# Performance work log

Hardware: AMD Instinct MI355X
Metric: run time of the kernel (lower is better)

## Reference

```python
import jax, jax.numpy as jnp
import numpy as np

K = 9          # kernel_size (number of KNN neighbours), dilation=1
SCALAR = 20.0  # scalar in _build_explain
EPS = 1e-10


def setup_inputs() -> dict:
    key = jax.random.key(0)
    ks = jax.random.split(key, 9)
    B, C, H, W = 16, 192, 28, 28
    Cout, r = 384, 16
    f = lambda k, s, sc: jax.random.normal(k, s, jnp.float32) * sc
    return {
        "x": f(ks[0], (B, C, H, W), 1.0),
        "w_edge": f(ks[1], (Cout, 2 * C), 0.05),  # 1x1 conv on concat[x_i, x_j-x_i]
        "b_edge": f(ks[2], (Cout,), 0.05),
        "w1": f(ks[3], (C // r, C), 0.1),          # CBAM channel MLP (shared)
        "b1": f(ks[4], (C // r,), 0.1),
        "w2": f(ks[5], (C, C // r), 0.1),
        "b2": f(ks[6], (C,), 0.1),
        "w_sp": f(ks[7], (1, 2, 7, 7), 0.1),       # CBAM spatial 7x7 conv
        "b_sp": f(ks[8], (1,), 0.1),
    }


def _cbam(x, w1, b1, w2, b2, w_sp, b_sp):
    # Standard CBAM: channel gate (avg+max pooled -> shared MLP -> sigmoid)
    # then spatial gate (channel mean/max -> 7x7 conv -> sigmoid).
    mlp = lambda v: jax.nn.relu(v @ w1.T + b1) @ w2.T + b2
    ch = jax.nn.sigmoid(mlp(x.mean((2, 3))) + mlp(x.max((2, 3))))
    x = x * ch[:, :, None, None]
    sp_in = jnp.stack([x.mean(1), x.max(1)], axis=1)  # (B,2,H,W)
    sp = jax.lax.conv_general_dilated(sp_in, w_sp, (1, 1), [(3, 3), (3, 3)])
    return x * jax.nn.sigmoid(sp + b_sp[None, :, None, None])


def _build_explain(att_x):
    B, C, H, W = att_x.shape
    a = jax.nn.softmax(att_x.reshape(B, C, H * W), axis=2)
    a = a / (a.max(axis=2, keepdims=True) + EPS)
    return (2.0 * a - 1.0) / (2.0 * SCALAR) + 1.0  # (B,C,N)


def _knn_idx(xf):
    # DenseDilatedKnnGraph: L2-normalize over channels, pairwise sq-dist, topk.
    xn = xf / jnp.maximum(jnp.linalg.norm(xf, axis=1, keepdims=True), 1e-12)
    xt = jnp.swapaxes(xn, 1, 2)                      # (B,N,C)
    sq = jnp.sum(xt * xt, axis=-1)                   # (B,N)
    dist = sq[:, :, None] - 2.0 * jnp.einsum("bnc,bmc->bnm", xt, xt) + sq[:, None, :]
    _, idx = jax.lax.top_k(-dist, K)                 # nn_idx = edge_index[0], (B,N,K)
    return idx


def reference(x, w_edge, b_edge, w1, b1, w2, b2, w_sp, b_sp):
    B, C, H, W = x.shape
    N = H * W
    xf = x.reshape(B, C, N)
    idx = _knn_idx(xf)                               # dynamic KNN graph (B,N,K)
    att = _build_explain(_cbam(x, w1, b1, w2, b2, w_sp, b_sp))
    xf = xf * att
    # EdgeConv2d: x_i = center (edge_index[1] is arange -> broadcast),
    # x_j gathered by neighbour indices.
    x_i = xf[:, :, :, None]                           # (B,C,N,1)
    x_e = jnp.broadcast_to(x_i, (B, C, N, K))
    i_e = jnp.broadcast_to(idx[:, None, :, :], (B, C, N, K))
    x_j = jnp.take_along_axis(x_e, i_e, axis=2)       # (B,C,N,K)
    feat = jnp.concatenate([x_e, x_j - x_i], axis=1)  # (B,2C,N,K)
    out = jnp.einsum("oc,bcnk->bonk", w_edge, feat) + b_edge[None, :, None, None]
    out = jax.nn.relu(out)                            # BasicConv: 1x1 conv + relu
    out = out.max(axis=-1)                            # max over neighbours (B,O,N)
    return out.reshape(B, -1, H, W)
```

## Files before the change

### kernel.cpp

```cpp
#include <hip/hip_runtime.h>
#include <math.h>

#define HW 784
#define Cc 192
#define Bb 16
#define CO 384
#define KK 9
#define OG 8

typedef __attribute__((ext_vector_type(8))) short bf16x8;
typedef __attribute__((ext_vector_type(4))) float f32x4;

__device__ __forceinline__ unsigned f2ord(float f){
  unsigned u = __float_as_uint(f);
  return (u & 0x80000000u) ? ~u : (u | 0x80000000u);
}

__device__ __forceinline__ unsigned short b16rne(float v){
  unsigned u = __float_as_uint(v);
  unsigned r = u + 0x7FFFu + ((u >> 16) & 1u);
  return (unsigned short)(r >> 16);
}

__global__ void k_chstats(const float* __restrict__ x, float* __restrict__ chm, float* __restrict__ chx){
  int wid = threadIdx.x >> 6, lane = threadIdx.x & 63;
  int r = blockIdx.x * 4 + wid;
  const float* row = x + (size_t)r * HW;
  float s = 0.f, m = -3.4e38f;
  for (int n = lane; n < HW; n += 64){ float v = row[n]; s += v; m = fmaxf(m, v); }
  for (int off = 32; off; off >>= 1){ s += __shfl_xor(s, off); m = fmaxf(m, __shfl_xor(m, off)); }
  if (lane == 0){ chm[r] = s / (float)HW; chx[r] = m; }
}

__global__ void k_mlp(const float* __restrict__ chm, const float* __restrict__ chx,
                      const float* __restrict__ w1, const float* __restrict__ b1,
                      const float* __restrict__ w2, const float* __restrict__ b2,
                      float* __restrict__ chv){
  int b = blockIdx.x, t = threadIdx.x;
  __shared__ float vm[Cc], vx[Cc], hp[2][12];
  if (t < Cc){ vm[t] = chm[b*Cc + t]; vx[t] = chx[b*Cc + t]; }
  __syncthreads();
  if (t < 24){
    int h = t % 12;
    const float* src = (t < 12) ? vm : vx;
    float a = b1[h];
    for (int c = 0; c < Cc; ++c) a += src[c] * w1[h*Cc + c];
    hp[t/12][h] = fmaxf(a, 0.f);
  }
  __syncthreads();
  if (t < Cc){
    float a = 2.f * b2[t];
    for (int h = 0; h < 12; ++h) a += (hp[0][h] + hp[1][h]) * w2[t*12 + h];
    chv[b*Cc + t] = 1.f / (1.f + expf(-a));
  }
}

__global__ void k_spin(const float* __restrict__ x, const float* __restrict__ chv,
                       float* __restrict__ amean, float* __restrict__ amax,
                       float* __restrict__ nrm){
  int b = blockIdx.x >> 2;
  int n = ((blockIdx.x & 3) << 8) + threadIdx.x;
  if (n >= HW) return;
  const float* xb = x + (size_t)b*Cc*HW + n;
  const float* cb = chv + b*Cc;
  float s = 0.f, m = -3.4e38f, sq = 0.f;
  for (int c = 0; c < Cc; ++c){
    float xv = xb[(size_t)c*HW];
    float v = xv * cb[c];
    s += v; m = fmaxf(m, v); sq += xv*xv;
  }
  amean[b*HW + n] = s / (float)Cc;
  amax[b*HW + n]  = m;
  nrm[b*HW + n]   = fmaxf(sqrtf(sq), 1e-12f);
}

__global__ void k_conv(const float* __restrict__ amean, const float* __restrict__ amax,
                       const float* __restrict__ wsp, const float* __restrict__ bsp,
                       float* __restrict__ satt){
  int b = blockIdx.x >> 2;
  int n = ((blockIdx.x & 3) << 8) + threadIdx.x;
  if (n >= HW) return;
  int yy = n / 28, xx = n % 28;
  float a = 0.f;
  for (int ky = 0; ky < 7; ++ky){
    int iy = yy + ky - 3; if (iy < 0 || iy >= 28) continue;
    for (int kx = 0; kx < 7; ++kx){
      int ix = xx + kx - 3; if (ix < 0 || ix >= 28) continue;
      int ii = b*HW + iy*28 + ix;
      a += amean[ii]*wsp[ky*7 + kx] + amax[ii]*wsp[49 + ky*7 + kx];
    }
  }
  satt[b*HW + n] = 1.f / (1.f + expf(-(a + bsp[0])));
}

__global__ void k_attstats(const float* __restrict__ x, const float* __restrict__ chv,
                           const float* __restrict__ satt,
                           float* __restrict__ vmaxA, float* __restrict__ invA){
  int wid = threadIdx.x >> 6, lane = threadIdx.x & 63;
  int r = blockIdx.x * 4 + wid;
  int b = r / Cc;
  const float* row = x + (size_t)r * HW;
  const float* sr = satt + b * HW;
  float ch = chv[r];
  float vv[13];
  float m = -3.4e38f;
  #pragma unroll
  for (int i = 0; i < 13; ++i){
    int n = lane + 64*i;
    vv[i] = (n < HW) ? (row[n] * ch) * sr[n] : -3.4e38f;
    m = fmaxf(m, vv[i]);
  }
  for (int off = 32; off; off >>= 1) m = fmaxf(m, __shfl_xor(m, off));
  float s = 0.f;
  #pragma unroll
  for (int i = 0; i < 13; ++i){
    int n = lane + 64*i;
    if (n < HW) s += expf(vv[i] - m);
  }
  for (int off = 32; off; off >>= 1) s += __shfl_xor(s, off);
  if (lane == 0){ vmaxA[r] = m; invA[r] = 1.f / (1.f + 1e-10f * s); }
}

__global__ __launch_bounds__(256) void k_cvt2(const float* __restrict__ x, const float* __restrict__ nrm,
                                              const float* __restrict__ chv, const float* __restrict__ satt,
                                              const float* __restrict__ vmaxA, const float* __restrict__ invA,
                                              unsigned short* __restrict__ Xnh, unsigned short* __restrict__ Xnl,
                                              unsigned short* __restrict__ XAh, unsigned short* __restrict__ XAl){
  int b = blockIdx.z, c0 = blockIdx.y*64, n0 = blockIdx.x*64;
  __shared__ float T[64][65];
  __shared__ float chs[64], vms[64], ivs[64];
  int t = threadIdx.x;
  int nl = (t & 15) * 4, cl = t >> 4;
  const float* xb = x + (size_t)b*Cc*HW;
  #pragma unroll
  for (int r = 0; r < 4; ++r){
    int c_loc = cl + r*16;
    int n = n0 + nl;
    float4 v = (n < HW) ? *(const float4*)(xb + (size_t)(c0 + c_loc)*HW + n) : make_float4(0,0,0,0);
    *(float4*)&T[c_loc][nl] = v;
  }
  if (t < 64){
    chs[t] = chv[b*Cc + c0 + t];
    vms[t] = vmaxA[b*Cc + c0 + t];
    ivs[t] = invA[b*Cc + c0 + t];
  }
  __syncthreads();
  int nr = t >> 2, q = t & 3;
  int n_g = n0 + nr;
  if (n_g >= HW) return;
  float nv = nrm[b*HW + n_g];
  float sr = satt[b*HW + n_g];
  unsigned int nh[8], nlw[8], ah[8], al[8];
  #pragma unroll
  for (int j = 0; j < 8; ++j){
    unsigned int parts[2][2];
    #pragma unroll
    for (int e = 0; e < 2; ++e){
      int cc_ = q*16 + 2*j + e;
      float v = T[cc_][nr];
      float xnv = v / nv;
      unsigned short h0 = b16rne(xnv);
      float l0 = xnv - __uint_as_float((unsigned)h0 << 16);
      parts[0][e] = (unsigned)h0 | ((unsigned)b16rne(l0) << 16);
      float vvv = (v * chs[cc_]) * sr;
      float ex = expf(vvv - vms[cc_]);
      float a = ex * ivs[cc_];
      float xav = v * ((2.f*a - 1.f)*0.025f + 1.f);
      unsigned short h1 = b16rne(xav);
      float l1 = xav - __uint_as_float((unsigned)h1 << 16);
      parts[1][e] = (unsigned)h1 | ((unsigned)b16rne(l1) << 16);
    }
    nh[j]  = (parts[0][0] & 0xFFFFu) | (parts[0][1] << 16);
    nlw[j] = (parts[0][0] >> 16)     | (parts[0][1] & 0xFFFF0000u);
    ah[j]  = (parts[1][0] & 0xFFFFu) | (parts[1][1] << 16);
    al[j]  = (parts[1][0] >> 16)     | (parts[1][1] & 0xFFFF0000u);
  }
  size_t base = ((size_t)b*HW + n_g)*Cc + c0 + q*16;
  *(uint4*)(Xnh + base)     = make_uint4(nh[0], nh[1], nh[2], nh[3]);
  *(uint4*)(Xnh + base + 8) = make_uint4(nh[4], nh[5], nh[6], nh[7]);
  *(uint4*)(Xnl + base)     = make_uint4(nlw[0], nlw[1], nlw[2], nlw[3]);
  *(uint4*)(Xnl + base + 8) = make_uint4(nlw[4], nlw[5], nlw[6], nlw[7]);
  *(uint4*)(XAh + base)     = make_uint4(ah[0], ah[1], ah[2], ah[3]);
  *(uint4*)(XAh + base + 8) = make_uint4(ah[4], ah[5], ah[6], ah[7]);
  *(uint4*)(XAl + base)     = make_uint4(al[0], al[1], al[2], al[3]);
  *(uint4*)(XAl + base + 8) = make_uint4(al[4], al[5], al[6], al[7]);
}

__global__ __launch_bounds__(256) void k_gram(const unsigned short* __restrict__ Xth,
                                              const unsigned short* __restrict__ Xtl,
                                              float* __restrict__ D){
  int b = blockIdx.z;
  int n0 = blockIdx.y*128, m0 = blockIdx.x*128;
  __shared__ unsigned short Als[8192];
  __shared__ unsigned short Bls[8192];
  int t = threadIdx.x, w = t >> 6, l = t & 63;
  int wr = w >> 1, wc = w & 1;
  f32x4 acc[4][4] = {};
  int nn = t >> 1, half = t & 1;
  size_t bb = (size_t)b*HW*Cc;
  int ra = n0 + nn; if (ra > HW-1) ra = HW-1;
  int rb = m0 + nn; if (rb > HW-1) rb = HW-1;

  for (int cc = 0; cc < 9; ++cc){
    int seg = cc/3, kc0 = (cc%3)*64;
    const unsigned short* As_ = (seg < 2 ? Xth : Xtl) + bb;
    const unsigned short* Bs_ = (seg == 1 ? Xtl : Xth) + bb;
    const uint4* ga = (const uint4*)(As_ + (size_t)ra*Cc + kc0 + half*32);
    const uint4* gb = (const uint4*)(Bs_ + (size_t)rb*Cc + kc0 + half*32);
    uint4 va0 = ga[0], va1 = ga[1], va2 = ga[2], va3 = ga[3];
    uint4 vb0 = gb[0], vb1 = gb[1], vb2 = gb[2], vb3 = gb[3];
    __syncthreads();
    int base = nn*128 + half*64;
    int sw = (nn & 7) << 4;
    *(uint4*)((char*)Als + ((base      ) ^ sw)) = va0;
    *(uint4*)((char*)Als + ((base + 16 ) ^ sw)) = va1;
    *(uint4*)((char*)Als + ((base + 32 ) ^ sw)) = va2;
    *(uint4*)((char*)Als + ((base + 48 ) ^ sw)) = va3;
    *(uint4*)((char*)Bls + ((base      ) ^ sw)) = vb0;
    *(uint4*)((char*)Bls + ((base + 16 ) ^ sw)) = vb1;
    *(uint4*)((char*)Bls + ((base + 32 ) ^ sw)) = vb2;
    *(uint4*)((char*)Bls + ((base + 48 ) ^ sw)) = vb3;
    __syncthreads();
    #pragma unroll
    for (int ks = 0; ks < 2; ++ks){
      bf16x8 af[4], bfr[4];
      int kb = ks*64 + (l >> 4)*16;
      #pragma unroll
      for (int mt = 0; mt < 4; ++mt){
        int rl = wr*64 + mt*16 + (l & 15);
        int off = (rl*128 + kb) ^ ((rl & 7) << 4);
        af[mt] = *(const bf16x8*)((const char*)Als + off);
      }
      #pragma unroll
      for (int nt = 0; nt < 4; ++nt){
        int cl2 = wc*64 + nt*16 + (l & 15);
        int off = (cl2*128 + kb) ^ ((cl2 & 7) << 4);
        bfr[nt] = *(const bf16x8*)((const char*)Bls + off);
      }
      #pragma unroll
      for (int mt = 0; mt < 4; ++mt)
        #pragma unroll
        for (int nt = 0; nt < 4; ++nt)
          acc[mt][nt] = __builtin_amdgcn_mfma_f32_16x16x32_bf16(af[mt], bfr[nt], acc[mt][nt], 0, 0, 0);
    }
  }
  #pragma unroll
  for (int mt = 0; mt < 4; ++mt){
    #pragma unroll
    for (int nt = 0; nt < 4; ++nt){
      int col = m0 + wc*64 + nt*16 + (l & 15);
      if (col >= HW) continue;
      int row0 = n0 + wr*64 + mt*16 + ((l >> 4) << 2);
      #pragma unroll
      for (int r = 0; r < 4; ++r){
        int row = row0 + r;
        if (row < HW) D[((size_t)b*HW + row)*HW + col] = -acc[mt][nt][r];
      }
    }
  }
}

__global__ __launch_bounds__(256) void k_select(const float* __restrict__ D, int* __restrict__ idxo){
  int wid = threadIdx.x >> 6, lane = threadIdx.x & 63;
  int row = blockIdx.x * 4 + wid;
  const float* Dr = D + (size_t)row * HW;
  float dvv[13]; int mvv[13];
  #pragma unroll
  for (int i = 0; i < 13; ++i){
    int m = lane + 64*i;
    dvv[i] = (m < HW) ? Dr[m] : 3.4e38f;
    mvv[i] = m;
  }
  for (int k = 0; k < KK; ++k){
    float bd = dvv[0]; int bi = 0;
    #pragma unroll
    for (int i = 1; i < 13; ++i) if (dvv[i] < bd){ bd = dvv[i]; bi = i; }
    unsigned long long key = ((unsigned long long)f2ord(bd) << 32) | (unsigned)mvv[bi];
    for (int off = 32; off; off >>= 1){
      unsigned long long o = __shfl_xor(key, off);
      if (o < key) key = o;
    }
    int wm = (int)(unsigned)(key & 0xffffffffu);
    if (lane == 0) idxo[(size_t)k*(Bb*HW) + row] = wm;
    if (mvv[bi] == wm) dvv[bi] = 3.4e38f;
  }
}

__global__ void k_wp(const float* __restrict__ we, unsigned short* __restrict__ Wph,
                     unsigned short* __restrict__ Wpl){
  int i = blockIdx.x*256 + threadIdx.x;
  if (i >= 768*Cc) return;
  int o = i / Cc, c = i % Cc;
  float v = (o < CO) ? (we[(size_t)o*384 + c] - we[(size_t)o*384 + Cc + c])
                     : we[(size_t)(o - CO)*384 + Cc + c];
  unsigned short h = b16rne(v);
  float lo = v - __uint_as_float((unsigned)h << 16);
  Wph[i] = h;
  Wpl[i] = b16rne(lo);
}

__global__ __launch_bounds__(256) void k_gemm2(const unsigned short* __restrict__ Wph,
                                               const unsigned short* __restrict__ Wpl,
                                               const unsigned short* __restrict__ XAh,
                                               const unsigned short* __restrict__ XAl,
                                               float* __restrict__ PQ){
  int b = blockIdx.z;
  int o0 = blockIdx.y*128, n0 = blockIdx.x*128;
  __shared__ unsigned short Als[8192];
  __shared__ unsigned short Bls[8192];
  int t = threadIdx.x, w = t >> 6, l = t & 63;
  int wr = w >> 1, wc = w & 1;
  f32x4 acc[4][4] = {};
  int nn = t >> 1, half = t & 1;
  size_t bx = (size_t)b*HW*Cc;
  int ra = o0 + nn;
  int rb = n0 + nn; if (rb > HW-1) rb = HW-1;

  for (int cc = 0; cc < 9; ++cc){
    int seg = cc/3, kc0 = (cc%3)*64;
    const unsigned short* As_ = (seg < 2 ? Wph : Wpl);
    const unsigned short* Bs_ = (seg == 1 ? XAl : XAh) + bx;
    const uint4* ga = (const uint4*)(As_ + (size_t)ra*Cc + kc0 + half*32);
    const uint4* gb = (const uint4*)(Bs_ + (size_t)rb*Cc + kc0 + half*32);
    uint4 va0 = ga[0], va1 = ga[1], va2 = ga[2], va3 = ga[3];
    uint4 vb0 = gb[0], vb1 = gb[1], vb2 = gb[2], vb3 = gb[3];
    __syncthreads();
    int base = nn*128 + half*64;
    int sw = (nn & 7) << 4;
    *(uint4*)((char*)Als + ((base      ) ^ sw)) = va0;
    *(uint4*)((char*)Als + ((base + 16 ) ^ sw)) = va1;
    *(uint4*)((char*)Als + ((base + 32 ) ^ sw)) = va2;
    *(uint4*)((char*)Als + ((base + 48 ) ^ sw)) = va3;
    *(uint4*)((char*)Bls + ((base      ) ^ sw)) = vb0;
    *(uint4*)((char*)Bls + ((base + 16 ) ^ sw)) = vb1;
    *(uint4*)((char*)Bls + ((base + 32 ) ^ sw)) = vb2;
    *(uint4*)((char*)Bls + ((base + 48 ) ^ sw)) = vb3;
    __syncthreads();
    #pragma unroll
    for (int ks = 0; ks < 2; ++ks){
      bf16x8 af[4], bfr[4];
      int kb = ks*64 + (l >> 4)*16;
      #pragma unroll
      for (int mt = 0; mt < 4; ++mt){
        int rl = wr*64 + mt*16 + (l & 15);
        int off = (rl*128 + kb) ^ ((rl & 7) << 4);
        af[mt] = *(const bf16x8*)((const char*)Als + off);
      }
      #pragma unroll
      for (int nt = 0; nt < 4; ++nt){
        int cl2 = wc*64 + nt*16 + (l & 15);
        int off = (cl2*128 + kb) ^ ((cl2 & 7) << 4);
        bfr[nt] = *(const bf16x8*)((const char*)Bls + off);
      }
      #pragma unroll
      for (int mt = 0; mt < 4; ++mt)
        #pragma unroll
        for (int nt = 0; nt < 4; ++nt)
          acc[mt][nt] = __builtin_amdgcn_mfma_f32_16x16x32_bf16(af[mt], bfr[nt], acc[mt][nt], 0, 0, 0);
    }
  }
  #pragma unroll
  for (int mt = 0; mt < 4; ++mt){
    #pragma unroll
    for (int nt = 0; nt < 4; ++nt){
      int col = n0 + wc*64 + nt*16 + (l & 15);
      if (col >= HW) continue;
      int row0 = o0 + wr*64 + mt*16 + ((l >> 4) << 2);
      #pragma unroll
      for (int r = 0; r < 4; ++r){
        PQ[((size_t)b*768 + row0 + r)*HW + col] = acc[mt][nt][r];
      }
    }
  }
}

__global__ __launch_bounds__(256) void k_edge(const float* __restrict__ PQ, const int* __restrict__ idx,
                                              const float* __restrict__ be, float* __restrict__ out){
  int bid = blockIdx.x;
  int b = bid / (CO/OG), og = bid % (CO/OG);
  int o0 = og * OG;
  __shared__ float Qls[OG][HW + 4];
  const float* Qbase = PQ + ((size_t)b*768 + CO + o0)*HW;
  int t = threadIdx.x;
  #pragma unroll
  for (int oo = 0; oo < OG; ++oo){
    if (t < 196) *(float4*)&Qls[oo][t*4] = *(const float4*)(Qbase + (size_t)oo*HW + t*4);
  }
  __syncthreads();
  const float* Pbase = PQ + ((size_t)b*768 + o0)*HW;
  float bev[OG];
  #pragma unroll
  for (int oo = 0; oo < OG; ++oo) bev[oo] = be[o0 + oo];
  for (int n = t; n < HW; n += 256){
    int ip[KK];
    #pragma unroll
    for (int k = 0; k < KK; ++k) ip[k] = idx[(size_t)k*(Bb*HW) + b*HW + n];
    float qm[OG];
    #pragma unroll
    for (int oo = 0; oo < OG; ++oo) qm[oo] = -3.4e38f;
    #pragma unroll
    for (int k = 0; k < KK; ++k){
      int j = ip[k];
      #pragma unroll
      for (int oo = 0; oo < OG; ++oo) qm[oo] = fmaxf(qm[oo], Qls[oo][j]);
    }
    #pragma unroll
    for (int oo = 0; oo < OG; ++oo){
      out[((size_t)b*CO + o0 + oo)*HW + n] = fmaxf(Pbase[(size_t)oo*HW + n] + bev[oo] + qm[oo], 0.f);
    }
  }
}

extern "C" void kernel_launch(void* const* d_in, const int* in_sizes, int n_in,
                              void* d_out, int out_size, void* d_ws, size_t ws_size,
                              hipStream_t stream){
  const float* x   = (const float*)d_in[0];
  const float* we  = (const float*)d_in[1];
  const float* be  = (const float*)d_in[2];
  const float* w1  = (const float*)d_in[3];
  const float* b1  = (const float*)d_in[4];
  const float* w2  = (const float*)d_in[5];
  const float* b2  = (const float*)d_in[6];
  const float* wsp = (const float*)d_in[7];
  const float* bsp = (const float*)d_in[8];
  float* out = (float*)d_out;

  float* ws    = (float*)d_ws;
  float* chm   = ws;
  float* chx   = chm + 3072;
  float* chv   = chx + 3072;
  float* vmaxA = chv + 3072;
  float* invA  = vmaxA + 3072;
  float* amean = invA + 3072;
  float* amax  = amean + 12544;
  float* satt  = amax + 12544;
  float* nrm   = satt + 12544;
  unsigned short* Wph = (unsigned short*)(nrm + 12544);
  unsigned short* Wpl = Wph + 147456;
  unsigned short* Xnh = Wpl + 147456;
  unsigned short* Xnl = Xnh + 2408448;
  unsigned short* XAh = Xnl + 2408448;
  unsigned short* XAl = XAh + 2408448;
  int*   idx   = (int*)(XAl + 2408448);
  float* D     = (float*)(idx + 112896);
  float* PQ    = D;

  k_chstats<<<768, 256, 0, stream>>>(x, chm, chx);
  k_mlp<<<16, 192, 0, stream>>>(chm, chx, w1, b1, w2, b2, chv);
  k_spin<<<64, 256, 0, stream>>>(x, chv, amean, amax, nrm);
  k_conv<<<64, 256, 0, stream>>>(amean, amax, wsp, bsp, satt);
  k_attstats<<<768, 256, 0, stream>>>(x, chv, satt, vmaxA, invA);
  k_cvt2<<<dim3(13, 3, 16), 256, 0, stream>>>(x, nrm, chv, satt, vmaxA, invA, Xnh, Xnl, XAh, XAl);
  k_gram<<<dim3(7, 7, 16), 256, 0, stream>>>(Xnh, Xnl, D);
  k_select<<<3136, 256, 0, stream>>>(D, idx);
  k_wp<<<576, 256, 0, stream>>>(we, Wph, Wpl);
  k_gemm2<<<dim3(7, 6, 16), 256, 0, stream>>>(Wph, Wpl, XAh, XAl, PQ);
  k_edge<<<Bb*(CO/OG), 256, 0, stream>>>(PQ, idx, be, out);
}
```

Before: 159.3 us.

## Merge gram and edge GEMM launches, fuse weight prep into convert, vectorise stats

```diff
diff --git a/kernel.cpp b/kernel.cpp
--- a/kernel.cpp
+++ b/kernel.cpp
@@ -25,9 +25,17 @@
 __global__ void k_chstats(const float* __restrict__ x, float* __restrict__ chm, float* __restrict__ chx){
   int wid = threadIdx.x >> 6, lane = threadIdx.x & 63;
   int r = blockIdx.x * 4 + wid;
-  const float* row = x + (size_t)r * HW;
+  const float4* row = (const float4*)(x + (size_t)r * HW);
   float s = 0.f, m = -3.4e38f;
-  for (int n = lane; n < HW; n += 64){ float v = row[n]; s += v; m = fmaxf(m, v); }
+  #pragma unroll
+  for (int i = 0; i < 4; ++i){
+    int f4 = lane + 64*i;
+    if (f4 < 196){
+      float4 v = row[f4];
+      s += v.x + v.y + v.z + v.w;
+      m = fmaxf(m, fmaxf(fmaxf(v.x, v.y), fmaxf(v.z, v.w)));
+    }
+  }
   for (int off = 32; off; off >>= 1){ s += __shfl_xor(s, off); m = fmaxf(m, __shfl_xor(m, off)); }
   if (lane == 0){ chm[r] = s / (float)HW; chx[r] = m; }
 }
@@ -99,37 +107,57 @@
   int wid = threadIdx.x >> 6, lane = threadIdx.x & 63;
   int r = blockIdx.x * 4 + wid;
   int b = r / Cc;
-  const float* row = x + (size_t)r * HW;
-  const float* sr = satt + b * HW;
+  const float4* row = (const float4*)(x + (size_t)r * HW);
+  const float4* sr  = (const float4*)(satt + b * HW);
   float ch = chv[r];
-  float vv[13];
+  float4 vv[4];
   float m = -3.4e38f;
   #pragma unroll
-  for (int i = 0; i < 13; ++i){
-    int n = lane + 64*i;
-    vv[i] = (n < HW) ? (row[n] * ch) * sr[n] : -3.4e38f;
-    m = fmaxf(m, vv[i]);
+  for (int i = 0; i < 4; ++i){
+    int f4 = lane + 64*i;
+    if (f4 < 196){
+      float4 xv = row[f4], sv = sr[f4];
+      vv[i].x = (xv.x * ch) * sv.x; vv[i].y = (xv.y * ch) * sv.y;
+      vv[i].z = (xv.z * ch) * sv.z; vv[i].w = (xv.w * ch) * sv.w;
+      m = fmaxf(m, fmaxf(fmaxf(vv[i].x, vv[i].y), fmaxf(vv[i].z, vv[i].w)));
+    }
   }
   for (int off = 32; off; off >>= 1) m = fmaxf(m, __shfl_xor(m, off));
   float s = 0.f;
   #pragma unroll
-  for (int i = 0; i < 13; ++i){
-    int n = lane + 64*i;
-    if (n < HW) s += expf(vv[i] - m);
+  for (int i = 0; i < 4; ++i){
+    int f4 = lane + 64*i;
+    if (f4 < 196){
+      s += expf(vv[i].x - m) + expf(vv[i].y - m) + expf(vv[i].z - m) + expf(vv[i].w - m);
+    }
   }
   for (int off = 32; off; off >>= 1) s += __shfl_xor(s, off);
   if (lane == 0){ vmaxA[r] = m; invA[r] = 1.f / (1.f + 1e-10f * s); }
 }
 
-__global__ __launch_bounds__(256) void k_cvt2(const float* __restrict__ x, const float* __restrict__ nrm,
-                                              const float* __restrict__ chv, const float* __restrict__ satt,
-                                              const float* __restrict__ vmaxA, const float* __restrict__ invA,
-                                              unsigned short* __restrict__ Xnh, unsigned short* __restrict__ Xnl,
-                                              unsigned short* __restrict__ XAh, unsigned short* __restrict__ XAl){
-  int b = blockIdx.z, c0 = blockIdx.y*64, n0 = blockIdx.x*64;
+__global__ __launch_bounds__(256) void k_cvt2wp(const float* __restrict__ x, const float* __restrict__ nrm,
+                                                const float* __restrict__ chv, const float* __restrict__ satt,
+                                                const float* __restrict__ vmaxA, const float* __restrict__ invA,
+                                                const float* __restrict__ we,
+                                                unsigned short* __restrict__ Xnh, unsigned short* __restrict__ Xnl,
+                                                unsigned short* __restrict__ XAh, unsigned short* __restrict__ XAl,
+                                                unsigned short* __restrict__ Wph, unsigned short* __restrict__ Wpl){
+  int bid = blockIdx.x, t = threadIdx.x;
+  if (bid >= 624){
+    int i = (bid - 624)*256 + t;
+    int o = i / Cc, c = i % Cc;
+    float v = (o < CO) ? (we[(size_t)o*384 + c] - we[(size_t)o*384 + Cc + c])
+                       : we[(size_t)(o - CO)*384 + Cc + c];
+    unsigned short h = b16rne(v);
+    float lo = v - __uint_as_float((unsigned)h << 16);
+    Wph[i] = h;
+    Wpl[i] = b16rne(lo);
+    return;
+  }
+  int xx = bid % 13, yy = (bid / 13) % 3, b = bid / 39;
+  int c0 = yy*64, n0 = xx*64;
   __shared__ float T[64][65];
   __shared__ float chs[64], vms[64], ivs[64];
-  int t = threadIdx.x;
   int nl = (t & 15) * 4, cl = t >> 4;
   const float* xb = x + (size_t)b*Cc*HW;
   #pragma unroll
@@ -186,25 +214,43 @@
   *(uint4*)(XAl + base + 8) = make_uint4(al[4], al[5], al[6], al[7]);
 }
 
-__global__ __launch_bounds__(256) void k_gram(const unsigned short* __restrict__ Xth,
-                                              const unsigned short* __restrict__ Xtl,
-                                              float* __restrict__ D){
-  int b = blockIdx.z;
-  int n0 = blockIdx.y*128, m0 = blockIdx.x*128;
+__global__ __launch_bounds__(256) void k_gramgemm(const unsigned short* __restrict__ Xnh,
+                                                  const unsigned short* __restrict__ Xnl,
+                                                  const unsigned short* __restrict__ Wph,
+                                                  const unsigned short* __restrict__ Wpl,
+                                                  const unsigned short* __restrict__ XAh,
+                                                  const unsigned short* __restrict__ XAl,
+                                                  float* __restrict__ D, float* __restrict__ PQ){
   __shared__ unsigned short Als[8192];
   __shared__ unsigned short Bls[8192];
+  int bid = blockIdx.x;
   int t = threadIdx.x, w = t >> 6, l = t & 63;
   int wr = w >> 1, wc = w & 1;
   f32x4 acc[4][4] = {};
   int nn = t >> 1, half = t & 1;
-  size_t bb = (size_t)b*HW*Cc;
-  int ra = n0 + nn; if (ra > HW-1) ra = HW-1;
-  int rb = m0 + nn; if (rb > HW-1) rb = HW-1;
+
+  bool isGram = bid < 784;
+  int b, r0, c0;
+  const unsigned short *A_h, *A_l, *B_h, *B_l;
+  if (isGram){
+    b = bid / 49; int rem = bid % 49;
+    c0 = (rem % 7) * 128; r0 = (rem / 7) * 128;
+    size_t bb = (size_t)b*HW*Cc;
+    A_h = Xnh + bb; A_l = Xnl + bb; B_h = Xnh + bb; B_l = Xnl + bb;
+  } else {
+    int id = bid - 784;
+    b = id / 42; int rem = id % 42;
+    c0 = (rem % 7) * 128; r0 = (rem / 7) * 128;
+    size_t bb = (size_t)b*HW*Cc;
+    A_h = Wph; A_l = Wpl; B_h = XAh + bb; B_l = XAl + bb;
+  }
+  int ra = r0 + nn; if (isGram && ra > HW-1) ra = HW-1;
+  int rb = c0 + nn; if (rb > HW-1) rb = HW-1;
 
   for (int cc = 0; cc < 9; ++cc){
     int seg = cc/3, kc0 = (cc%3)*64;
-    const unsigned short* As_ = (seg < 2 ? Xth : Xtl) + bb;
-    const unsigned short* Bs_ = (seg == 1 ? Xtl : Xth) + bb;
+    const unsigned short* As_ = (seg < 2 ? A_h : A_l);
+    const unsigned short* Bs_ = (seg == 1 ? B_l : B_h);
     const uint4* ga = (const uint4*)(As_ + (size_t)ra*Cc + kc0 + half*32);
     const uint4* gb = (const uint4*)(Bs_ + (size_t)rb*Cc + kc0 + half*32);
     uint4 va0 = ga[0], va1 = ga[1], va2 = ga[2], va3 = ga[3];
@@ -244,17 +290,33 @@
           acc[mt][nt] = __builtin_amdgcn_mfma_f32_16x16x32_bf16(af[mt], bfr[nt], acc[mt][nt], 0, 0, 0);
     }
   }
-  #pragma unroll
-  for (int mt = 0; mt < 4; ++mt){
-    #pragma unroll
-    for (int nt = 0; nt < 4; ++nt){
-      int col = m0 + wc*64 + nt*16 + (l & 15);
-      if (col >= HW) continue;
-      int row0 = n0 + wr*64 + mt*16 + ((l >> 4) << 2);
-      #pragma unroll
-      for (int r = 0; r < 4; ++r){
-        int row = row0 + r;
-        if (row < HW) D[((size_t)b*HW + row)*HW + col] = -acc[mt][nt][r];
+  if (isGram){
+    #pragma unroll
+    for (int mt = 0; mt < 4; ++mt){
+      #pragma unroll
+      for (int nt = 0; nt < 4; ++nt){
+        int col = c0 + wc*64 + nt*16 + (l & 15);
+        if (col >= HW) continue;
+        int row0 = r0 + wr*64 + mt*16 + ((l >> 4) << 2);
+        #pragma unroll
+        for (int r = 0; r < 4; ++r){
+          int row = row0 + r;
+          if (row < HW) D[((size_t)b*HW + row)*HW + col] = -acc[mt][nt][r];
+        }
+      }
+    }
+  } else {
+    #pragma unroll
+    for (int mt = 0; mt < 4; ++mt){
+      #pragma unroll
+      for (int nt = 0; nt < 4; ++nt){
+        int col = c0 + wc*64 + nt*16 + (l & 15);
+        if (col >= HW) continue;
+        int row0 = r0 + wr*64 + mt*16 + ((l >> 4) << 2);
+        #pragma unroll
+        for (int r = 0; r < 4; ++r){
+          PQ[((size_t)b*768 + row0 + r)*HW + col] = acc[mt][nt][r];
+        }
       }
     }
   }
@@ -283,94 +345,6 @@
     int wm = (int)(unsigned)(key & 0xffffffffu);
     if (lane == 0) idxo[(size_t)k*(Bb*HW) + row] = wm;
     if (mvv[bi] == wm) dvv[bi] = 3.4e38f;
-  }
-}
-
-__global__ void k_wp(const float* __restrict__ we, unsigned short* __restrict__ Wph,
-                     unsigned short* __restrict__ Wpl){
-  int i = blockIdx.x*256 + threadIdx.x;
-  if (i >= 768*Cc) return;
-  int o = i / Cc, c = i % Cc;
-  float v = (o < CO) ? (we[(size_t)o*384 + c] - we[(size_t)o*384 + Cc + c])
-                     : we[(size_t)(o - CO)*384 + Cc + c];
-  unsigned short h = b16rne(v);
-  float lo = v - __uint_as_float((unsigned)h << 16);
-  Wph[i] = h;
-  Wpl[i] = b16rne(lo);
-}
-
-__global__ __launch_bounds__(256) void k_gemm2(const unsigned short* __restrict__ Wph,
-                                               const unsigned short* __restrict__ Wpl,
-                                               const unsigned short* __restrict__ XAh,
-                                               const unsigned short* __restrict__ XAl,
-                                               float* __restrict__ PQ){
-  int b = blockIdx.z;
-  int o0 = blockIdx.y*128, n0 = blockIdx.x*128;
-  __shared__ unsigned short Als[8192];
-  __shared__ unsigned short Bls[8192];
-  int t = threadIdx.x, w = t >> 6, l = t & 63;
-  int wr = w >> 1, wc = w & 1;
-  f32x4 acc[4][4] = {};
-  int nn = t >> 1, half = t & 1;
-  size_t bx = (size_t)b*HW*Cc;
-  int ra = o0 + nn;
-  int rb = n0 + nn; if (rb > HW-1) rb = HW-1;
-
-  for (int cc = 0; cc < 9; ++cc){
-    int seg = cc/3, kc0 = (cc%3)*64;
-    const unsigned short* As_ = (seg < 2 ? Wph : Wpl);
-    const unsigned short* Bs_ = (seg == 1 ? XAl : XAh) + bx;
-    const uint4* ga = (const uint4*)(As_ + (size_t)ra*Cc + kc0 + half*32);
-    const uint4* gb = (const uint4*)(Bs_ + (size_t)rb*Cc + kc0 + half*32);
-    uint4 va0 = ga[0], va1 = ga[1], va2 = ga[2], va3 = ga[3];
-    uint4 vb0 = gb[0], vb1 = gb[1], vb2 = gb[2], vb3 = gb[3];
-    __syncthreads();
-    int base = nn*128 + half*64;
-    int sw = (nn & 7) << 4;
-    *(uint4*)((char*)Als + ((base      ) ^ sw)) = va0;
-    *(uint4*)((char*)Als + ((base + 16 ) ^ sw)) = va1;
-    *(uint4*)((char*)Als + ((base + 32 ) ^ sw)) = va2;
-    *(uint4*)((char*)Als + ((base + 48 ) ^ sw)) = va3;
-    *(uint4*)((char*)Bls + ((base      ) ^ sw)) = vb0;
-    *(uint4*)((char*)Bls + ((base + 16 ) ^ sw)) = vb1;
-    *(uint4*)((char*)Bls + ((base + 32 ) ^ sw)) = vb2;
-    *(uint4*)((char*)Bls + ((base + 48 ) ^ sw)) = vb3;
-    __syncthreads();
-    #pragma unroll
-    for (int ks = 0; ks < 2; ++ks){
-      bf16x8 af[4], bfr[4];
-      int kb = ks*64 + (l >> 4)*16;
-      #pragma unroll
-      for (int mt = 0; mt < 4; ++mt){
-        int rl = wr*64 + mt*16 + (l & 15);
-        int off = (rl*128 + kb) ^ ((rl & 7) << 4);
-        af[mt] = *(const bf16x8*)((const char*)Als + off);
-      }
-      #pragma unroll
-      for (int nt = 0; nt < 4; ++nt){
-        int cl2 = wc*64 + nt*16 + (l & 15);
-        int off = (cl2*128 + kb) ^ ((cl2 & 7) << 4);
-        bfr[nt] = *(const bf16x8*)((const char*)Bls + off);
-      }
-      #pragma unroll
-      for (int mt = 0; mt < 4; ++mt)
-        #pragma unroll
-        for (int nt = 0; nt < 4; ++nt)
-          acc[mt][nt] = __builtin_amdgcn_mfma_f32_16x16x32_bf16(af[mt], bfr[nt], acc[mt][nt], 0, 0, 0);
-    }
-  }
-  #pragma unroll
-  for (int mt = 0; mt < 4; ++mt){
-    #pragma unroll
-    for (int nt = 0; nt < 4; ++nt){
-      int col = n0 + wc*64 + nt*16 + (l & 15);
-      if (col >= HW) continue;
-      int row0 = o0 + wr*64 + mt*16 + ((l >> 4) << 2);
-      #pragma unroll
-      for (int r = 0; r < 4; ++r){
-        PQ[((size_t)b*768 + row0 + r)*HW + col] = acc[mt][nt][r];
-      }
-    }
   }
 }
 
@@ -443,17 +417,16 @@
   unsigned short* XAl = XAh + 2408448;
   int*   idx   = (int*)(XAl + 2408448);
   float* D     = (float*)(idx + 112896);
-  float* PQ    = D;
+  float* PQ    = D + 9834496;
 
   k_chstats<<<768, 256, 0, stream>>>(x, chm, chx);
   k_mlp<<<16, 192, 0, stream>>>(chm, chx, w1, b1, w2, b2, chv);
   k_spin<<<64, 256, 0, stream>>>(x, chv, amean, amax, nrm);
   k_conv<<<64, 256, 0, stream>>>(amean, amax, wsp, bsp, satt);
   k_attstats<<<768, 256, 0, stream>>>(x, chv, satt, vmaxA, invA);
-  k_cvt2<<<dim3(13, 3, 16), 256, 0, stream>>>(x, nrm, chv, satt, vmaxA, invA, Xnh, Xnl, XAh, XAl);
-  k_gram<<<dim3(7, 7, 16), 256, 0, stream>>>(Xnh, Xnl, D);
+  k_cvt2wp<<<1200, 256, 0, stream>>>(x, nrm, chv, satt, vmaxA, invA, we,
+                                     Xnh, Xnl, XAh, XAl, Wph, Wpl);
+  k_gramgemm<<<1456, 256, 0, stream>>>(Xnh, Xnl, Wph, Wpl, XAh, XAl, D, PQ);
   k_select<<<3136, 256, 0, stream>>>(D, idx);
-  k_wp<<<576, 256, 0, stream>>>(we, Wph, Wpl);
-  k_gemm2<<<dim3(7, 6, 16), 256, 0, stream>>>(Wph, Wpl, XAh, XAl, PQ);
   k_edge<<<Bb*(CO/OG), 256, 0, stream>>>(PQ, idx, be, out);
 }
```

New measurement: 146.0 us. 8.3% less time.
